# Performance work log

Measured on AMD Instinct MI355X. Metric: run time of the kernel, lower is better.

## Reference

```python
import jax, jax.numpy as jnp
import numpy as np

COMMITMENT_COST = 0.25
NUM_EMBEDDINGS = 1024
EMBEDDING_DIM = 64


def setup_inputs() -> dict:
    key = jax.random.key(0)
    k1, k2 = jax.random.split(key)
    x = jax.random.normal(k1, (32, 64, 64, 64), dtype=jnp.float32)
    embeddings = jax.random.normal(k2, (EMBEDDING_DIM, NUM_EMBEDDINGS), dtype=jnp.float32)
    return {"x": x, "embeddings": embeddings}


def reference(x, embeddings):
    # x: [..., D], embeddings: [D, K]
    flat = jnp.reshape(x, (-1, EMBEDDING_DIM))                       # [N, D]
    # squared euclidean distances via ||a||^2 - 2 a.e + ||e||^2      # [N, K]
    distances = (jnp.sum(flat * flat, axis=1, keepdims=True)
                 - 2.0 * (flat @ embeddings)
                 + jnp.sum(embeddings * embeddings, axis=0, keepdims=True))
    flat_indices = jnp.argmax(-distances, axis=1)                    # [N]
    encodings = jax.nn.one_hot(flat_indices, NUM_EMBEDDINGS, dtype=distances.dtype)  # [N, K]
    encoding_indices = jnp.reshape(flat_indices, x.shape[:-1])
    # gather codebook rows: embeddings.T[idx]
    quantized = jnp.take(embeddings.T, encoding_indices, axis=0)     # same shape as x
    e_latent_loss = jnp.mean((jax.lax.stop_gradient(quantized) - x) ** 2)
    q_latent_loss = jnp.mean((quantized - jax.lax.stop_gradient(x)) ** 2)
    loss = q_latent_loss + COMMITMENT_COST * e_latent_loss
    quantized_st = x + jax.lax.stop_gradient(quantized - x)          # straight-through
    avg_probs = jnp.mean(encodings, axis=0)                          # [K]
    perplexity = jnp.exp(-jnp.sum(avg_probs * jnp.log(avg_probs + 1e-10)))
    return quantized_st, loss, perplexity, encodings, encoding_indices, distances
```

## Files before the change

### kernel.cpp

```cpp
#include <hip/hip_runtime.h>
#include <hip/hip_bf16.h>
#include <math.h>

#define NROWS 131072
#define DDIM  64
#define KCODE 1024
#define TAU_B 0.008f

#define OFF_Q    0L
#define OFF_LOSS 8388608L
#define OFF_PERP 8388609L
#define OFF_ENC  8388610L
#define OFF_IDX  (OFF_ENC + 134217728L)
#define OFF_DIST (OFF_IDX + 131072L)

#define WS_ENORM 0L
#define WS_ET    1024L
#define WS_EBPH  66560L
#define WS_EBPL  99328L
#define WS_IDX   132096L
#define WS_CNT   263168L
#define WS_PART  395268L

typedef short bf16x8 __attribute__((ext_vector_type(8)));
typedef float f32x4  __attribute__((ext_vector_type(4)));
typedef float f32x2  __attribute__((ext_vector_type(2)));
typedef _Float16 f16x4v __attribute__((ext_vector_type(4)));

__device__ inline unsigned short f2bf(float f) {
    unsigned u = __float_as_uint(f);
    unsigned r = (u + 0x7fffu + ((u >> 16) & 1u)) >> 16;
    return (unsigned short)r;
}
__device__ inline float bf2f(unsigned short h) {
    return __uint_as_float(((unsigned)h) << 16);
}
__device__ inline int dswz16(int i) { return i ^ (((i >> 12) & 3) << 3); }

__global__ __launch_bounds__(256) void k1a_prep(const float* __restrict__ e,
                                                float* __restrict__ enorm,
                                                float* __restrict__ eT,
                                                int* __restrict__ cnt) {
    int k = blockIdx.x * 256 + threadIdx.x;
    float s = 0.f;
    #pragma unroll 8
    for (int d = 0; d < DDIM; ++d) {
        float v = e[(size_t)d * KCODE + k];
        s = fmaf(v, v, s);
        eT[(size_t)k * DDIM + d] = v;
    }
    enorm[k] = s;
    cnt[k] = 0;
}

__global__ __launch_bounds__(128) void k1b_pack(const float* __restrict__ e,
                                                unsigned short* __restrict__ ebph,
                                                unsigned short* __restrict__ ebpl) {
    const int gct = blockIdx.x;
    const int ks  = threadIdx.x >> 6;
    const int l   = threadIdx.x & 63;
    const int col = (gct << 4) | (l & 15);
    const int kb  = (ks << 5) + ((l >> 4) << 3);
    const size_t ob = ((size_t)((gct << 1) | ks) * 64 + l) * 8;
    #pragma unroll
    for (int j = 0; j < 8; ++j) {
        float f = e[(size_t)(kb + j) * KCODE + col];
        unsigned short h = f2bf(f);
        float lo = f - bf2f(h);
        ebph[ob + j] = h;
        ebpl[ob + j] = f2bf(lo);
    }
}

__global__ __launch_bounds__(256, 4) void kA_dist(const float* __restrict__ x,
                                                  const float* __restrict__ e,
                                                  const unsigned short* __restrict__ ebph,
                                                  const unsigned short* __restrict__ ebpl,
                                                  const float* __restrict__ enorm,
                                                  float* __restrict__ dist,
                                                  int* __restrict__ idxarr,
                                                  int* __restrict__ cnt,
                                                  float* __restrict__ partials) {
    __shared__ __align__(16) _Float16 dtH[16384];
    __shared__ float hd[2];
    __shared__ short xh[16 * 64];
    __shared__ short xl[16 * 64];
    __shared__ float xn[16];
    __shared__ float wm1[4][16], wm2[4][16];
    __shared__ int   wi1[4][16];
    __shared__ float ps[16];
    __shared__ int   sidx[16];
    __shared__ int   nearmask;
    __shared__ float xsh[DDIM];
    __shared__ double wbv[4];
    __shared__ int    wbi[4];

    const int tid  = threadIdx.x;
    const int lane = tid & 63;
    const int w    = tid >> 6;
    const int rowbase = blockIdx.x * 16;

    {
        if (tid == 0) nearmask = 0;
        float4 v = ((const float4*)(x + (size_t)rowbase * DDIM))[tid];
        int fi = tid * 4, r = fi >> 6, c = fi & 63;
        float fv[4] = {v.x, v.y, v.z, v.w};
        short hv[4], lv[4];
        #pragma unroll
        for (int q = 0; q < 4; ++q) {
            unsigned short hh = f2bf(fv[q]);
            hv[q] = (short)hh;
            lv[q] = (short)f2bf(fv[q] - bf2f(hh));
        }
        *(short4*)&xh[r * 64 + c] = make_short4(hv[0], hv[1], hv[2], hv[3]);
        *(short4*)&xl[r * 64 + c] = make_short4(lv[0], lv[1], lv[2], lv[3]);
        float s4 = fmaf(v.x, v.x, fmaf(v.y, v.y, fmaf(v.z, v.z, v.w * v.w)));
        #pragma unroll
        for (int m = 1; m < 16; m <<= 1) s4 += __shfl_xor(s4, m);
        if ((lane & 15) == 0) xn[r] = s4;
    }
    __syncthreads();

    const int arow = lane & 15, akb = (lane >> 4) << 3;
    bf16x8 ah0 = *(const bf16x8*)&xh[arow * 64 + akb];
    bf16x8 ah1 = *(const bf16x8*)&xh[arow * 64 + 32 + akb];
    bf16x8 al0 = *(const bf16x8*)&xl[arow * 64 + akb];
    bf16x8 al1 = *(const bf16x8*)&xl[arow * 64 + 32 + akb];

    const int wr   = (lane >> 4) << 2;
    const int colb = (w << 8) | (lane & 15);
    float xnv[4];
    #pragma unroll
    for (int r = 0; r < 4; ++r) xnv[r] = xn[wr + r];
    float env[16];
    #pragma unroll
    for (int ct = 0; ct < 16; ++ct) env[ct] = enorm[colb + (ct << 4)];

    float m1[4], m2[4];
    int   i1[4];
    #pragma unroll
    for (int r = 0; r < 4; ++r) { m1[r] = 3.4e38f; m2[r] = 3.4e38f; i1[r] = 1 << 30; }

    #pragma unroll 4
    for (int ct = 0; ct < 16; ++ct) {
        const int gct = (w << 4) | ct;
        const size_t bo = ((size_t)(gct << 1) * 64 + lane) * 8;
        bf16x8 bh0 = *(const bf16x8*)(ebph + bo);
        bf16x8 bh1 = *(const bf16x8*)(ebph + bo + 512);
        bf16x8 bl0 = *(const bf16x8*)(ebpl + bo);
        bf16x8 bl1 = *(const bf16x8*)(ebpl + bo + 512);

        f32x4 d = {0.f, 0.f, 0.f, 0.f};
        d = __builtin_amdgcn_mfma_f32_16x16x32_bf16(ah0, bh0, d, 0, 0, 0);
        d = __builtin_amdgcn_mfma_f32_16x16x32_bf16(ah1, bh1, d, 0, 0, 0);
        d = __builtin_amdgcn_mfma_f32_16x16x32_bf16(ah0, bl0, d, 0, 0, 0);
        d = __builtin_amdgcn_mfma_f32_16x16x32_bf16(ah1, bl1, d, 0, 0, 0);
        d = __builtin_amdgcn_mfma_f32_16x16x32_bf16(al0, bh0, d, 0, 0, 0);
        d = __builtin_amdgcn_mfma_f32_16x16x32_bf16(al1, bh1, d, 0, 0, 0);

        const int col = colb + (ct << 4);
        #pragma unroll
        for (int r = 0; r < 4; ++r) {
            float o = fmaf(-2.f, d[r], xnv[r] + env[ct]);
            if (o < m1[r]) { m2[r] = m1[r]; m1[r] = o; i1[r] = col; }
            else if (o < m2[r]) m2[r] = o;
            const int fl = ((wr + r) << 10) + col;
            if (fl >= 2) dtH[dswz16(fl - 2)] = (_Float16)o;
            else         hd[fl] = o;
        }
    }

    #pragma unroll
    for (int m = 1; m < 16; m <<= 1) {
        #pragma unroll
        for (int r = 0; r < 4; ++r) {
            float om1 = __shfl_xor(m1[r], m);
            int   oi1 = __shfl_xor(i1[r], m);
            float om2 = __shfl_xor(m2[r], m);
            if (om1 < m1[r] || (om1 == m1[r] && oi1 < i1[r])) {
                m2[r] = fminf(m1[r], om2); m1[r] = om1; i1[r] = oi1;
            } else {
                m2[r] = fminf(m2[r], om1);
            }
        }
    }
    if ((lane & 15) == 0) {
        #pragma unroll
        for (int r = 0; r < 4; ++r) {
            wm1[w][wr + r] = m1[r];
            wm2[w][wr + r] = m2[r];
            wi1[w][wr + r] = i1[r];
        }
    }
    __syncthreads();
    if (tid < 16) {
        float bm1 = wm1[0][tid], bm2 = wm2[0][tid];
        int   bi  = wi1[0][tid];
        #pragma unroll
        for (int wv = 1; wv < 4; ++wv) {
            float om1 = wm1[wv][tid], om2 = wm2[wv][tid];
            int   oi  = wi1[wv][tid];
            if (om1 < bm1 || (om1 == bm1 && oi < bi)) {
                bm2 = fminf(bm1, om2); bm1 = om1; bi = oi;
            } else {
                bm2 = fminf(bm2, om1);
            }
        }
        sidx[tid] = bi;
        ps[tid]   = bm1;
        if (bm2 - bm1 < TAU_B) atomicOr(&nearmask, 1 << tid);
    }
    __syncthreads();

    {
        float* dbase = dist + ((size_t)rowbase << 10);
        #pragma unroll
        for (int j = 0; j < 16; ++j) {
            const int s = (j << 8) + tid;
            if (s < 4095) {
                const int i0 = s << 2;
                const int iw = dswz16(i0);
                f16x4v h = *(const f16x4v*)&dtH[iw];
                f32x4 v = {(float)h[0], (float)h[1], (float)h[2], (float)h[3]};
                *(f32x4*)(dbase + 2 + i0) = v;
            }
        }
        if (tid == 255) {
            const int it = dswz16(16380);
            *(f32x2*)(dbase)         = (f32x2){hd[0], hd[1]};
            *(f32x2*)(dbase + 16382) = (f32x2){(float)dtH[it], (float)dtH[it + 1]};
        }
    }

    if (nearmask) {
        for (int mrow = nearmask; mrow; mrow &= (mrow - 1)) {
            const int r = __ffs(mrow) - 1;
            if (tid < DDIM) xsh[tid] = x[(size_t)(rowbase + r) * DDIM + tid];
            __syncthreads();
            const int k0 = tid * 4;
            double dd[4] = {0.0, 0.0, 0.0, 0.0};
            for (int d = 0; d < DDIM; ++d) {
                double xd = (double)xsh[d];
                float4 ev = *(const float4*)(e + (size_t)d * KCODE + k0);
                double t0 = xd - (double)ev.x; dd[0] = fma(t0, t0, dd[0]);
                double t1 = xd - (double)ev.y; dd[1] = fma(t1, t1, dd[1]);
                double t2 = xd - (double)ev.z; dd[2] = fma(t2, t2, dd[2]);
                double t3 = xd - (double)ev.w; dd[3] = fma(t3, t3, dd[3]);
            }
            double best = dd[0]; int bidx = k0;
            #pragma unroll
            for (int c = 1; c < 4; ++c)
                if (dd[c] < best) { best = dd[c]; bidx = k0 + c; }
            #pragma unroll
            for (int m = 1; m < 64; m <<= 1) {
                double ob = __shfl_xor(best, m);
                int    oi = __shfl_xor(bidx, m);
                if (ob < best || (ob == best && oi < bidx)) { best = ob; bidx = oi; }
            }
            if (lane == 0) { wbv[w] = best; wbi[w] = bidx; }
            __syncthreads();
            if (tid == 0) {
                double bb = wbv[0]; int bi = wbi[0];
                #pragma unroll
                for (int wv = 1; wv < 4; ++wv)
                    if (wbv[wv] < bb || (wbv[wv] == bb && wbi[wv] < bi)) {
                        bb = wbv[wv]; bi = wbi[wv];
                    }
                sidx[r] = bi; ps[r] = (float)bb;
            }
            __syncthreads();
        }
    }

    if (tid < 16) {
        const int idx = sidx[tid];
        idxarr[rowbase + tid] = idx;
        atomicAdd(cnt + idx, 1);
    }
    if (tid == 64) {
        float s = 0.f;
        #pragma unroll
        for (int j = 0; j < 16; ++j) s += ps[j];
        partials[blockIdx.x] = s;
    }
}

__global__ __launch_bounds__(256) void kC_final(const float* __restrict__ eT,
                                                const int* __restrict__ idxarr,
                                                float* __restrict__ outq,
                                                float* __restrict__ enc,
                                                float* __restrict__ outidx) {
    __shared__ int sidx[64];
    const int tid = threadIdx.x;
    const int rowbase = blockIdx.x * 64;

    if (tid < 64) {
        const int grow = rowbase + tid;
        const int idx = idxarr[grow];
        sidx[tid] = idx;
        outidx[grow] = (float)idx;
    }

    #pragma unroll
    for (int it = 0; it < 4; ++it) {
        const int row = (it << 4) + (tid >> 4);
        const int grow = rowbase + row;
        const int idx = idxarr[grow];
        f32x4 ev = *(const f32x4*)(eT + (size_t)idx * DDIM + ((tid & 15) << 2));
        *((f32x4*)(outq + ((size_t)grow << 6)) + (tid & 15)) = ev;
    }

    float* ebase = enc + ((size_t)rowbase << 10);
    const f32x4 z4 = {0.f, 0.f, 0.f, 0.f};
    #pragma unroll 9
    for (int j = 0; j < 63; ++j) {
        const int s = (j << 8) + tid;
        *(f32x4*)(ebase + 2 + (s << 2)) = z4;
    }
    if (tid < 255) {
        const int s = (63 << 8) + tid;
        *(f32x4*)(ebase + 2 + (s << 2)) = z4;
    }
    if (tid == 255) {
        *(f32x2*)(ebase)         = (f32x2){0.f, 0.f};
        *(f32x2*)(ebase + 65534) = (f32x2){0.f, 0.f};
    }

    __syncthreads();
    if (tid < 64) {
        ebase[((size_t)tid << 10) + sidx[tid]] = 1.0f;
    }
}

__global__ __launch_bounds__(256) void k6_scalar(const float* __restrict__ partials,
                                                 const int* __restrict__ cnt,
                                                 float* __restrict__ outloss,
                                                 float* __restrict__ outperp) {
    __shared__ double sd[256];
    const int tid = threadIdx.x;
    double s = 0.0;
    for (int i = tid; i < 8192; i += 256) s += (double)partials[i];
    sd[tid] = s;
    __syncthreads();
    for (int st = 128; st > 0; st >>= 1) {
        if (tid < st) sd[tid] += sd[tid + st];
        __syncthreads();
    }
    const double total = sd[0];
    __syncthreads();
    double h = 0.0;
    for (int k = tid; k < KCODE; k += 256) {
        double p = (double)cnt[k] / (double)NROWS;
        h -= p * log(p + 1e-10);
    }
    sd[tid] = h;
    __syncthreads();
    for (int st = 128; st > 0; st >>= 1) {
        if (tid < st) sd[tid] += sd[tid + st];
        __syncthreads();
    }
    if (tid == 0) {
        *outloss = (float)(total * 1.25 / (double)((long)NROWS * DDIM));
        *outperp = (float)exp(sd[0]);
    }
}

extern "C" void kernel_launch(void* const* d_in, const int* in_sizes, int n_in,
                              void* d_out, int out_size, void* d_ws, size_t ws_size,
                              hipStream_t stream) {
    const float* x = (const float*)d_in[0];
    const float* e = (const float*)d_in[1];
    float* out = (float*)d_out;

    float* ws_f = (float*)d_ws;
    float* enorm   = ws_f + WS_ENORM;
    float* eT      = ws_f + WS_ET;
    unsigned short* ebph = (unsigned short*)(ws_f + WS_EBPH);
    unsigned short* ebpl = (unsigned short*)(ws_f + WS_EBPL);
    int*   idxarr  = (int*)(ws_f + WS_IDX);
    int*   cnt     = (int*)(ws_f + WS_CNT);
    float* partials= ws_f + WS_PART;

    float* outq    = out + OFF_Q;
    float* outloss = out + OFF_LOSS;
    float* outperp = out + OFF_PERP;
    float* enc     = out + OFF_ENC;
    float* outidx  = out + OFF_IDX;
    float* dist    = out + OFF_DIST;

    hipLaunchKernelGGL(k1a_prep, dim3(4),    dim3(256), 0, stream, e, enorm, eT, cnt);
    hipLaunchKernelGGL(k1b_pack, dim3(64),   dim3(128), 0, stream, e, ebph, ebpl);
    hipLaunchKernelGGL(kA_dist,  dim3(8192), dim3(256), 0, stream, x, e, ebph, ebpl, enorm,
                       dist, idxarr, cnt, partials);
    hipLaunchKernelGGL(kC_final, dim3(2048), dim3(256), 0, stream, eT, idxarr, outq, enc, outidx);
    hipLaunchKernelGGL(k6_scalar,dim3(1),    dim3(256), 0, stream, partials, cnt, outloss, outperp);
}
```

Before: 341.1 us.

## Fuse one-hot, gather and index output into the distance kernel

Removes the separate finalization kernel. The distance kernel now zero-fills its 16-row slice of the one-hot encoding matrix inside the MFMA loop, then writes the 1.0 entries, the float indices and the gathered quantized rows directly. This drops a kernel launch and the round trip of the index array through global memory. It also lets the large encoding writes overlap with the matrix math. In exchange, the distance kernel takes on extra store traffic and register pressure.

```diff
diff --git a/kernel.cpp b/kernel.cpp
--- a/kernel.cpp
+++ b/kernel.cpp
@@ -18,7 +18,6 @@
 #define WS_ET    1024L
 #define WS_EBPH  66560L
 #define WS_EBPL  99328L
-#define WS_IDX   132096L
 #define WS_CNT   263168L
 #define WS_PART  395268L
 
@@ -72,15 +71,18 @@
     }
 }
 
-__global__ __launch_bounds__(256, 4) void kA_dist(const float* __restrict__ x,
-                                                  const float* __restrict__ e,
-                                                  const unsigned short* __restrict__ ebph,
-                                                  const unsigned short* __restrict__ ebpl,
-                                                  const float* __restrict__ enorm,
-                                                  float* __restrict__ dist,
-                                                  int* __restrict__ idxarr,
-                                                  int* __restrict__ cnt,
-                                                  float* __restrict__ partials) {
+__global__ __launch_bounds__(256, 4) void kA_fused(const float* __restrict__ x,
+                                                   const float* __restrict__ e,
+                                                   const unsigned short* __restrict__ ebph,
+                                                   const unsigned short* __restrict__ ebpl,
+                                                   const float* __restrict__ enorm,
+                                                   const float* __restrict__ eT,
+                                                   float* __restrict__ dist,
+                                                   float* __restrict__ enc,
+                                                   float* __restrict__ outq,
+                                                   float* __restrict__ outidx,
+                                                   int* __restrict__ cnt,
+                                                   float* __restrict__ partials) {
     __shared__ __align__(16) _Float16 dtH[16384];
     __shared__ float hd[2];
     __shared__ short xh[16 * 64];
@@ -99,6 +101,7 @@
     const int lane = tid & 63;
     const int w    = tid >> 6;
     const int rowbase = blockIdx.x * 16;
+    float* ebase = enc + ((size_t)blockIdx.x << 14);
 
     {
         if (tid == 0) nearmask = 0;
@@ -140,6 +143,8 @@
     int   i1[4];
     #pragma unroll
     for (int r = 0; r < 4; ++r) { m1[r] = 3.4e38f; m2[r] = 3.4e38f; i1[r] = 1 << 30; }
+
+    const f32x4 z4 = {0.f, 0.f, 0.f, 0.f};
 
     #pragma unroll 4
     for (int ct = 0; ct < 16; ++ct) {
@@ -149,6 +154,16 @@
         bf16x8 bh1 = *(const bf16x8*)(ebph + bo + 512);
         bf16x8 bl0 = *(const bf16x8*)(ebpl + bo);
         bf16x8 bl1 = *(const bf16x8*)(ebpl + bo + 512);
+
+        {
+            const int s = (ct << 8) + tid;
+            if (s < 4095) {
+                *(f32x4*)(ebase + 2 + (s << 2)) = z4;
+            } else {
+                *(f32x2*)(ebase)         = (f32x2){0.f, 0.f};
+                *(f32x2*)(ebase + 16382) = (f32x2){0.f, 0.f};
+            }
+        }
 
         f32x4 d = {0.f, 0.f, 0.f, 0.f};
         d = __builtin_amdgcn_mfma_f32_16x16x32_bf16(ah0, bh0, d, 0, 0, 0);
@@ -274,61 +289,21 @@
 
     if (tid < 16) {
         const int idx = sidx[tid];
-        idxarr[rowbase + tid] = idx;
+        ebase[((size_t)tid << 10) + idx] = 1.0f;
+        outidx[rowbase + tid] = (float)idx;
         atomicAdd(cnt + idx, 1);
+    }
+    {
+        const int r = tid >> 4, c = tid & 15;
+        const int idx = sidx[r];
+        f32x4 ev = *(const f32x4*)(eT + (size_t)idx * DDIM + (c << 2));
+        *((f32x4*)(outq + ((size_t)(rowbase + r) << 6)) + c) = ev;
     }
     if (tid == 64) {
         float s = 0.f;
         #pragma unroll
         for (int j = 0; j < 16; ++j) s += ps[j];
         partials[blockIdx.x] = s;
-    }
-}
-
-__global__ __launch_bounds__(256) void kC_final(const float* __restrict__ eT,
-                                                const int* __restrict__ idxarr,
-                                                float* __restrict__ outq,
-                                                float* __restrict__ enc,
-                                                float* __restrict__ outidx) {
-    __shared__ int sidx[64];
-    const int tid = threadIdx.x;
-    const int rowbase = blockIdx.x * 64;
-
-    if (tid < 64) {
-        const int grow = rowbase + tid;
-        const int idx = idxarr[grow];
-        sidx[tid] = idx;
-        outidx[grow] = (float)idx;
-    }
-
-    #pragma unroll
-    for (int it = 0; it < 4; ++it) {
-        const int row = (it << 4) + (tid >> 4);
-        const int grow = rowbase + row;
-        const int idx = idxarr[grow];
-        f32x4 ev = *(const f32x4*)(eT + (size_t)idx * DDIM + ((tid & 15) << 2));
-        *((f32x4*)(outq + ((size_t)grow << 6)) + (tid & 15)) = ev;
-    }
-
-    float* ebase = enc + ((size_t)rowbase << 10);
-    const f32x4 z4 = {0.f, 0.f, 0.f, 0.f};
-    #pragma unroll 9
-    for (int j = 0; j < 63; ++j) {
-        const int s = (j << 8) + tid;
-        *(f32x4*)(ebase + 2 + (s << 2)) = z4;
-    }
-    if (tid < 255) {
-        const int s = (63 << 8) + tid;
-        *(f32x4*)(ebase + 2 + (s << 2)) = z4;
-    }
-    if (tid == 255) {
-        *(f32x2*)(ebase)         = (f32x2){0.f, 0.f};
-        *(f32x2*)(ebase + 65534) = (f32x2){0.f, 0.f};
-    }
-
-    __syncthreads();
-    if (tid < 64) {
-        ebase[((size_t)tid << 10) + sidx[tid]] = 1.0f;
     }
 }
 
@@ -377,7 +352,6 @@
     float* eT      = ws_f + WS_ET;
     unsigned short* ebph = (unsigned short*)(ws_f + WS_EBPH);
     unsigned short* ebpl = (unsigned short*)(ws_f + WS_EBPL);
-    int*   idxarr  = (int*)(ws_f + WS_IDX);
     int*   cnt     = (int*)(ws_f + WS_CNT);
     float* partials= ws_f + WS_PART;
 
@@ -390,8 +364,7 @@
 
     hipLaunchKernelGGL(k1a_prep, dim3(4),    dim3(256), 0, stream, e, enorm, eT, cnt);
     hipLaunchKernelGGL(k1b_pack, dim3(64),   dim3(128), 0, stream, e, ebph, ebpl);
-    hipLaunchKernelGGL(kA_dist,  dim3(8192), dim3(256), 0, stream, x, e, ebph, ebpl, enorm,
-                       dist, idxarr, cnt, partials);
-    hipLaunchKernelGGL(kC_final, dim3(2048), dim3(256), 0, stream, eT, idxarr, outq, enc, outidx);
+    hipLaunchKernelGGL(kA_fused, dim3(8192), dim3(256), 0, stream, x, e, ebph, ebpl, enorm,
+                       eT, dist, enc, outq, outidx, cnt, partials);
     hipLaunchKernelGGL(k6_scalar,dim3(1),    dim3(256), 0, stream, partials, cnt, outloss, outperp);
 }
```

After: 283.3 us. 17.0% less time.
